# Performance work log

Hardware: AMD Instinct MI355X
Metric: run time of the kernel (lower is better)

The kernel has to match this reference:

```python
import jax, jax.numpy as jnp
import numpy as np

SHAPE = (192, 192, 192)


def _trilinear_sample(img, z, y, x):
    # img: [B,C,D,H,W]; z,y,x: [B,D,H,W] absolute voxel coords (align_corners=True,
    # zero padding outside the volume, matching F.grid_sample defaults in vroc).
    B, C, D, H, W = img.shape
    imgf = img.reshape(B, C, -1)
    z0 = jnp.floor(z); y0 = jnp.floor(y); x0 = jnp.floor(x)
    wz = z - z0; wy = y - y0; wx = x - x0
    z0i = z0.astype(jnp.int32); y0i = y0.astype(jnp.int32); x0i = x0.astype(jnp.int32)
    z1i = z0i + 1; y1i = y0i + 1; x1i = x0i + 1

    def gather(iz, iy, ix):
        valid = ((iz >= 0) & (iz < D) & (iy >= 0) & (iy < H) & (ix >= 0) & (ix < W))
        lin = ((jnp.clip(iz, 0, D - 1) * H + jnp.clip(iy, 0, H - 1)) * W
               + jnp.clip(ix, 0, W - 1)).reshape(B, 1, -1)
        v = jnp.take_along_axis(imgf, jnp.broadcast_to(lin, (B, C, D * H * W)), axis=2)
        return v.reshape(B, C, D, H, W) * valid.reshape(B, 1, D, H, W).astype(img.dtype)

    def w(a, b, c):
        return (a * b * c)[:, None]  # [B,1,D,H,W]

    out = (gather(z0i, y0i, x0i) * w(1 - wz, 1 - wy, 1 - wx)
           + gather(z0i, y0i, x1i) * w(1 - wz, 1 - wy, wx)
           + gather(z0i, y1i, x0i) * w(1 - wz, wy, 1 - wx)
           + gather(z0i, y1i, x1i) * w(1 - wz, wy, wx)
           + gather(z1i, y0i, x0i) * w(wz, 1 - wy, 1 - wx)
           + gather(z1i, y0i, x1i) * w(wz, 1 - wy, wx)
           + gather(z1i, y1i, x0i) * w(wz, wy, 1 - wx)
           + gather(z1i, y1i, x1i) * w(wz, wy, wx))
    return out


def _warp(moving_image, vector_field):
    # SpatialTransformer: identity grid + displacement (voxel units), trilinear sample.
    B, C, D, H, W = moving_image.shape
    dt = moving_image.dtype
    gz, gy, gx = jnp.meshgrid(jnp.arange(D, dtype=dt), jnp.arange(H, dtype=dt),
                              jnp.arange(W, dtype=dt), indexing='ij')
    z = gz[None] + vector_field[:, 0]
    y = gy[None] + vector_field[:, 1]
    x = gx[None] + vector_field[:, 2]
    return _trilinear_sample(moving_image, z, y, x)


def setup_inputs() -> dict:
    key = jax.random.key(0)
    k1, k2, k3, k4 = jax.random.split(key, 4)
    D, H, W = SHAPE
    moving_image = jax.random.normal(k1, (1, 1, D, H, W), dtype=jnp.float32)
    vector_field = jax.random.normal(k2, (1, 3, D, H, W), dtype=jnp.float32) * 3.0
    fixed_image = jax.random.normal(k3, (1, 1, D, H, W), dtype=jnp.float32)
    fixed_image_mask = jax.random.randint(k4, (1, 1, D, H, W), 0, 2).astype(bool)
    return {"moving_image": moving_image, "vector_field": vector_field,
            "fixed_image": fixed_image, "fixed_image_mask": fixed_image_mask}


def reference(moving_image, vector_field, fixed_image, fixed_image_mask):
    warped = _warp(moving_image, vector_field)
    m = fixed_image_mask.astype(warped.dtype)
    sq = (warped - fixed_image) ** 2
    # F.mse_loss(warped[mask], fixed[mask]) == mean of squared diff over masked voxels
    return jnp.sum(sq * m) / jnp.maximum(jnp.sum(m), 1.0)
```

## Files before the change

### kernel.cpp

```cpp
#include <hip/hip_runtime.h>
#include <hip/hip_fp16.h>

#define DD 192
#define HH 192
#define WW 192
#define NVOX (DD * HH * WW)

#define RSX 32
#define RSY 33
#define RSZ 33
#define ROWD 16
#define SLABD (RSY * ROWD)
#define RTOTH (RSX * RSY * RSZ)
#define RTOTD (RTOTH / 2)
#define MAXO (RTOTD - SLABD - ROWD - 2)
#define NCHUNK (RTOTH / 8)
#define CHSLAB (RSY * 4)
#define NT 1024
#define NTILE 1728
#define GRID 256

#define AS1 __attribute__((address_space(1)))
#define AS3 __attribute__((address_space(3)))

__global__ __launch_bounds__(256) void conv_fp16(
    const float4* __restrict__ in, int4* __restrict__ out)
{
    const int i = blockIdx.x * 256 + threadIdx.x;
    const float4 a = in[2 * i];
    const float4 b = in[2 * i + 1];
    __half2 h0 = __floats2half2_rn(a.x, a.y);
    __half2 h1 = __floats2half2_rn(a.z, a.w);
    __half2 h2 = __floats2half2_rn(b.x, b.y);
    __half2 h3 = __floats2half2_rn(b.z, b.w);
    int4 o;
    o.x = *(int*)&h0; o.y = *(int*)&h1; o.z = *(int*)&h2; o.w = *(int*)&h3;
    out[i] = o;
}

struct Streams { float4 dz, dy, dx, f; int4 m; };

__device__ __forceinline__ void tile_coords(int n, int& tx, int& ty, int& tz) {
    tx = n / 144;
    const int r = n - tx * 144;
    ty = r / 12;
    tz = r - ty * 12;
}

__device__ __forceinline__ void stage_tile(
    const ushort* __restrict__ movh, const ushort* __restrict__ zbuf,
    uint* sbufd, int x_lo, int y_lo, int z_lo, int tid)
{
    ushort* sbuf = (ushort*)sbufd;
    #pragma unroll
    for (int i = 0; i < 5; ++i) {
        const int q = tid + i * NT;
        if (q < NCHUNK) {
            const int rz = q / CHSLAB;
            const int rem = q - rz * CHSLAB;
            const int ry = rem >> 2;
            const int k  = rem & 3;
            const int gz = z_lo + rz, gy = y_lo + ry, gx = x_lo + 8 * k;
            const bool valid = ((unsigned)gz < DD) & ((unsigned)gy < HH) &
                               ((unsigned)gx < WW);
            const ushort* src = valid ? (movh + ((gz * HH + gy) * WW + gx)) : zbuf;
            const int qb = i * NT + (tid & ~63);
            __builtin_amdgcn_global_load_lds((AS1 void*)src,
                                             (AS3 void*)(sbuf + 8 * qb), 16, 0, 0);
        }
    }
}

__device__ __forceinline__ Streams prefetch_streams(
    const float* __restrict__ vf, const float* __restrict__ fix,
    const int* __restrict__ mask, int base)
{
    Streams s;
    s.dz = *(const float4*)(vf + base);
    s.dy = *(const float4*)(vf + NVOX + base);
    s.dx = *(const float4*)(vf + 2 * NVOX + base);
    s.f  = *(const float4*)(fix + base);
    s.m  = *(const int4*)(mask + base);
    return s;
}

__device__ __forceinline__ void sample_accum(
    const uint* sdw, const float* __restrict__ mov,
    int gz, int gy, int gx, float dz, float dy, float dx,
    float f, int m, int x_lo, int y_lo, int z_lo,
    float& sq, float& cnt)
{
    const float z = (float)gz + dz, y = (float)gy + dy, x = (float)gx + dx;
    const float z0f = floorf(z), y0f = floorf(y), x0f = floorf(x);
    const float wz = z - z0f, wy = y - y0f, wx = x - x0f;
    const int z0 = (int)z0f, y0 = (int)y0f, x0 = (int)x0f;
    const int z0l = z0 - z_lo, y0l = y0 - y_lo, x0l = x0 - x_lo;
    const bool inbox = ((unsigned)z0l < RSZ - 1) & ((unsigned)y0l < RSY - 1) &
                       ((unsigned)x0l < RSX - 1);

    float v000, v001, v010, v011, v100, v101, v110, v111;
    if (inbox) {
        const int o = z0l * SLABD + y0l * ROWD + (x0l >> 1);
        const bool odd = (x0l & 1) != 0;
        const uint a00 = sdw[o];
        const uint b00 = sdw[o + 1];
        const uint a01 = sdw[o + ROWD];
        const uint b01 = sdw[o + ROWD + 1];
        const uint a10 = sdw[o + SLABD];
        const uint b10 = sdw[o + SLABD + 1];
        const uint a11 = sdw[o + SLABD + ROWD];
        const uint b11 = sdw[o + SLABD + ROWD + 1];
        auto pr = [&](uint A, uint B, float& l, float& r) {
            const float2 fa = __half22float2(*(const __half2*)&A);
            const float fb = __low2float(*(const __half2*)&B);
            l = odd ? fa.y : fa.x;
            r = odd ? fb   : fa.y;
        };
        pr(a00, b00, v000, v001);
        pr(a01, b01, v010, v011);
        pr(a10, b10, v100, v101);
        pr(a11, b11, v110, v111);
    } else {
        const int z1 = z0 + 1, y1 = y0 + 1, x1 = x0 + 1;
        const bool zi0 = (unsigned)z0 < DD, zi1 = (unsigned)z1 < DD;
        const bool yi0 = (unsigned)y0 < HH, yi1 = (unsigned)y1 < HH;
        const bool xi0 = (unsigned)x0 < WW, xi1 = (unsigned)x1 < WW;
        auto ld = [&](int iz, int iy, int ix, bool ok) -> float {
            return ok ? mov[(iz * HH + iy) * WW + ix] : 0.0f;
        };
        v000 = ld(z0, y0, x0, zi0 & yi0 & xi0);
        v001 = ld(z0, y0, x1, zi0 & yi0 & xi1);
        v010 = ld(z0, y1, x0, zi0 & yi1 & xi0);
        v011 = ld(z0, y1, x1, zi0 & yi1 & xi1);
        v100 = ld(z1, y0, x0, zi1 & yi0 & xi0);
        v101 = ld(z1, y0, x1, zi1 & yi0 & xi1);
        v110 = ld(z1, y1, x0, zi1 & yi1 & xi0);
        v111 = ld(z1, y1, x1, zi1 & yi1 & xi1);
    }

    const float c00 = v000 + (v001 - v000) * wx;
    const float c01 = v010 + (v011 - v010) * wx;
    const float c10 = v100 + (v101 - v100) * wx;
    const float c11 = v110 + (v111 - v110) * wx;
    const float c0 = c00 + (c01 - c00) * wy;
    const float c1 = c10 + (c11 - c10) * wy;
    const float warped = c0 + (c1 - c0) * wz;

    const float mm = (m != 0) ? 1.0f : 0.0f;
    const float diff = warped - f;
    sq += diff * diff * mm;
    cnt += mm;
}

__global__ __launch_bounds__(NT) void warp_mse_persist(
    const ushort* __restrict__ movh,
    const float* __restrict__ mov,
    const float* __restrict__ vf,
    const float* __restrict__ fix,
    const int* __restrict__ mask,
    const ushort* __restrict__ zbuf,
    float* __restrict__ acc,
    float* __restrict__ out)
{
    __shared__ uint sbufd[2][RTOTD];
    __shared__ float s_sq[16], s_cnt[16];

    const int tid = threadIdx.x;
    const int b = blockIdx.x;
    const int start = b * 6 + min(b, 192);
    const int cnt_t = 6 + (b < 192 ? 1 : 0);

    const int lxg = (tid & 3) * 4;
    const int ly  = (tid >> 2) & 15;
    const int lz  = tid >> 6;

    float sq = 0.0f, cntm = 0.0f;

    int tx, ty, tz;
    tile_coords(start, tx, ty, tz);
    stage_tile(movh, zbuf, sbufd[0], tx * 16 - 8, ty * 16 - 8, tz * 16 - 8, tid);
    Streams S0 = prefetch_streams(vf, fix, mask,
        ((tz * 16 + lz) * HH + ty * 16 + ly) * WW + tx * 16 + lxg);
    __syncthreads();

    for (int k = 0; k < cnt_t; ++k) {
        const int cur = k & 1;
        Streams S1 = S0;
        if (k + 1 < cnt_t) {
            int nx, ny, nz;
            tile_coords(start + k + 1, nx, ny, nz);
            stage_tile(movh, zbuf, sbufd[cur ^ 1],
                       nx * 16 - 8, ny * 16 - 8, nz * 16 - 8, tid);
            S1 = prefetch_streams(vf, fix, mask,
                ((nz * 16 + lz) * HH + ny * 16 + ly) * WW + nx * 16 + lxg);
        }

        int cx, cy, cz;
        tile_coords(start + k, cx, cy, cz);
        const int x_lo = cx * 16 - 8, y_lo = cy * 16 - 8, z_lo = cz * 16 - 8;
        const int gz = cz * 16 + lz, gy = cy * 16 + ly, gx0 = cx * 16 + lxg;
        const uint* sdw = sbufd[cur];

        sample_accum(sdw, mov, gz, gy, gx0,     S0.dz.x, S0.dy.x, S0.dx.x,
                     S0.f.x, S0.m.x, x_lo, y_lo, z_lo, sq, cntm);
        sample_accum(sdw, mov, gz, gy, gx0 + 1, S0.dz.y, S0.dy.y, S0.dx.y,
                     S0.f.y, S0.m.y, x_lo, y_lo, z_lo, sq, cntm);
        sample_accum(sdw, mov, gz, gy, gx0 + 2, S0.dz.z, S0.dy.z, S0.dx.z,
                     S0.f.z, S0.m.z, x_lo, y_lo, z_lo, sq, cntm);
        sample_accum(sdw, mov, gz, gy, gx0 + 3, S0.dz.w, S0.dy.w, S0.dx.w,
                     S0.f.w, S0.m.w, x_lo, y_lo, z_lo, sq, cntm);

        __syncthreads();
        S0 = S1;
    }

    #pragma unroll
    for (int off = 32; off > 0; off >>= 1) {
        sq   += __shfl_down(sq, off, 64);
        cntm += __shfl_down(cntm, off, 64);
    }
    const int lane = tid & 63;
    const int wid = tid >> 6;
    if (lane == 0) { s_sq[wid] = sq; s_cnt[wid] = cntm; }
    __syncthreads();
    if (tid == 0) {
        float bsq = 0.0f, bcnt = 0.0f;
        #pragma unroll
        for (int i = 0; i < 16; ++i) { bsq += s_sq[i]; bcnt += s_cnt[i]; }
        atomicAdd(&acc[0], bsq);
        atomicAdd(&acc[1], bcnt);
        __threadfence();
        const unsigned old = atomicAdd((unsigned*)&acc[2], 1u);
        if (old == GRID - 1) {
            __threadfence();
            const float s = atomicAdd(&acc[0], 0.0f);
            const float c = atomicAdd(&acc[1], 0.0f);
            out[0] = s / fmaxf(c, 1.0f);
        }
    }
}

__global__ __launch_bounds__(256) void warp_mse_simple(
    const float* __restrict__ mov, const float* __restrict__ vf,
    const float* __restrict__ fix, const int* __restrict__ mask,
    float* __restrict__ acc)
{
    const int idx = blockIdx.x * 256 + threadIdx.x;
    float sq = 0.0f, cnt = 0.0f;
    if (idx < NVOX) {
        const int w = idx % WW;
        const int t = idx / WW;
        const int h = t % HH;
        const int d = t / HH;
        const float z = (float)d + vf[idx];
        const float y = (float)h + vf[NVOX + idx];
        const float x = (float)w + vf[2 * NVOX + idx];
        const float z0f = floorf(z), y0f = floorf(y), x0f = floorf(x);
        const float wz = z - z0f, wy = y - y0f, wx = x - x0f;
        const int z0 = (int)z0f, y0 = (int)y0f, x0 = (int)x0f;
        const int z1 = z0 + 1, y1 = y0 + 1, x1 = x0 + 1;
        const bool zi0 = (unsigned)z0 < DD, zi1 = (unsigned)z1 < DD;
        const bool yi0 = (unsigned)y0 < HH, yi1 = (unsigned)y1 < HH;
        const bool xi0 = (unsigned)x0 < WW, xi1 = (unsigned)x1 < WW;
        auto ld = [&](int iz, int iy, int ix, bool ok) -> float {
            return ok ? mov[(iz * HH + iy) * WW + ix] : 0.0f;
        };
        const float v000 = ld(z0, y0, x0, zi0 & yi0 & xi0);
        const float v001 = ld(z0, y0, x1, zi0 & yi0 & xi1);
        const float v010 = ld(z0, y1, x0, zi0 & yi1 & xi0);
        const float v011 = ld(z0, y1, x1, zi0 & yi1 & xi1);
        const float v100 = ld(z1, y0, x0, zi1 & yi0 & xi0);
        const float v101 = ld(z1, y0, x1, zi1 & yi0 & xi1);
        const float v110 = ld(z1, y1, x0, zi1 & yi1 & xi0);
        const float v111 = ld(z1, y1, x1, zi1 & yi1 & xi1);
        const float c00 = v000 + (v001 - v000) * wx;
        const float c01 = v010 + (v011 - v010) * wx;
        const float c10 = v100 + (v101 - v100) * wx;
        const float c11 = v110 + (v111 - v110) * wx;
        const float c0 = c00 + (c01 - c00) * wy;
        const float c1 = c10 + (c11 - c10) * wy;
        const float warped = c0 + (c1 - c0) * wz;
        const float m = (mask[idx] != 0) ? 1.0f : 0.0f;
        const float diff = warped - fix[idx];
        sq = diff * diff * m;
        cnt = m;
    }
    #pragma unroll
    for (int off = 32; off > 0; off >>= 1) {
        sq  += __shfl_down(sq, off, 64);
        cnt += __shfl_down(cnt, off, 64);
    }
    __shared__ float s_sq[4], s_cnt[4];
    const int lane = threadIdx.x & 63, wid = threadIdx.x >> 6;
    if (lane == 0) { s_sq[wid] = sq; s_cnt[wid] = cnt; }
    __syncthreads();
    if (threadIdx.x == 0) {
        atomicAdd(&acc[0], s_sq[0] + s_sq[1] + s_sq[2] + s_sq[3]);
        atomicAdd(&acc[1], s_cnt[0] + s_cnt[1] + s_cnt[2] + s_cnt[3]);
    }
}

__global__ void warp_mse_finalize(const float* __restrict__ acc, float* __restrict__ out) {
    out[0] = acc[0] / fmaxf(acc[1], 1.0f);
}

extern "C" void kernel_launch(void* const* d_in, const int* in_sizes, int n_in,
                              void* d_out, int out_size, void* d_ws, size_t ws_size,
                              hipStream_t stream) {
    const float* mov  = (const float*)d_in[0];
    const float* vf   = (const float*)d_in[1];
    const float* fix  = (const float*)d_in[2];
    const int*   mask = (const int*)d_in[3];
    float* acc = (float*)d_ws;
    float* out = (float*)d_out;

    hipMemsetAsync(d_ws, 0, 256, stream);

    const size_t need = 256 + (size_t)NVOX * 2;
    if (ws_size >= need) {
        ushort* movh = (ushort*)((char*)d_ws + 256);
        const ushort* zbuf = (const ushort*)((char*)d_ws + 64);
        conv_fp16<<<NVOX / (256 * 8), 256, 0, stream>>>(
            (const float4*)mov, (int4*)movh);
        warp_mse_persist<<<GRID, NT, 0, stream>>>(movh, mov, vf, fix, mask,
                                                  zbuf, acc, out);
    } else {
        warp_mse_simple<<<(NVOX + 255) / 256, 256, 0, stream>>>(mov, vf, fix, mask, acc);
        warp_mse_finalize<<<1, 1, 0, stream>>>(acc, out);
    }
}
```

Before: 246.0 us.

## Single-buffer LDS tile with 512-thread blocks for higher occupancy and locality

Halves the block size to 512 threads, with each thread handling two z-slices of a tile, and drops the LDS double buffer in favour of one tile buffer. Launch bounds now request four blocks per CU and the grid grows to 512 blocks. Blocks are remapped so that neighbouring blocks take interleaved tiles. Streaming loads of the displacement field, fixed image and mask become nontemporal. More resident blocks should hide latency better, but staging is no longer overlapped with compute within a block and now needs an extra barrier per tile.

```diff
diff --git a/kernel.cpp b/kernel.cpp
--- a/kernel.cpp
+++ b/kernel.cpp
@@ -13,15 +13,18 @@
 #define SLABD (RSY * ROWD)
 #define RTOTH (RSX * RSY * RSZ)
 #define RTOTD (RTOTH / 2)
-#define MAXO (RTOTD - SLABD - ROWD - 2)
 #define NCHUNK (RTOTH / 8)
 #define CHSLAB (RSY * 4)
-#define NT 1024
+#define NT 512
+#define NROUND ((NCHUNK + NT - 1) / NT)
 #define NTILE 1728
-#define GRID 256
+#define GRID 512
 
 #define AS1 __attribute__((address_space(1)))
 #define AS3 __attribute__((address_space(3)))
+
+typedef float f32x4 __attribute__((ext_vector_type(4)));
+typedef int   i32x4 __attribute__((ext_vector_type(4)));
 
 __global__ __launch_bounds__(256) void conv_fp16(
     const float4* __restrict__ in, int4* __restrict__ out)
@@ -38,7 +41,7 @@
     out[i] = o;
 }
 
-struct Streams { float4 dz, dy, dx, f; int4 m; };
+struct Streams { f32x4 dz, dy, dx, f; i32x4 m; };
 
 __device__ __forceinline__ void tile_coords(int n, int& tx, int& ty, int& tz) {
     tx = n / 144;
@@ -53,7 +56,7 @@
 {
     ushort* sbuf = (ushort*)sbufd;
     #pragma unroll
-    for (int i = 0; i < 5; ++i) {
+    for (int i = 0; i < NROUND; ++i) {
         const int q = tid + i * NT;
         if (q < NCHUNK) {
             const int rz = q / CHSLAB;
@@ -76,11 +79,11 @@
     const int* __restrict__ mask, int base)
 {
     Streams s;
-    s.dz = *(const float4*)(vf + base);
-    s.dy = *(const float4*)(vf + NVOX + base);
-    s.dx = *(const float4*)(vf + 2 * NVOX + base);
-    s.f  = *(const float4*)(fix + base);
-    s.m  = *(const int4*)(mask + base);
+    s.dz = __builtin_nontemporal_load((const f32x4*)(vf + base));
+    s.dy = __builtin_nontemporal_load((const f32x4*)(vf + NVOX + base));
+    s.dx = __builtin_nontemporal_load((const f32x4*)(vf + 2 * NVOX + base));
+    s.f  = __builtin_nontemporal_load((const f32x4*)(fix + base));
+    s.m  = __builtin_nontemporal_load((const i32x4*)(mask + base));
     return s;
 }
 
@@ -152,7 +155,7 @@
     cnt += mm;
 }
 
-__global__ __launch_bounds__(NT) void warp_mse_persist(
+__global__ __launch_bounds__(NT, 4) void warp_mse_persist(
     const ushort* __restrict__ movh,
     const float* __restrict__ mov,
     const float* __restrict__ vf,
@@ -162,13 +165,14 @@
     float* __restrict__ acc,
     float* __restrict__ out)
 {
-    __shared__ uint sbufd[2][RTOTD];
-    __shared__ float s_sq[16], s_cnt[16];
+    __shared__ uint sbufd[RTOTD];
+    __shared__ float s_sq[8], s_cnt[8];
 
     const int tid = threadIdx.x;
-    const int b = blockIdx.x;
-    const int start = b * 6 + min(b, 192);
-    const int cnt_t = 6 + (b < 192 ? 1 : 0);
+    const int b0 = blockIdx.x;
+    const int b = ((b0 & 7) << 6) | (b0 >> 3);
+    const int start = 3 * b + 3 * (b >> 3) + min(b & 7, 3);
+    const int cnt_t = 3 + ((b & 7) < 3 ? 1 : 0);
 
     const int lxg = (tid & 3) * 4;
     const int ly  = (tid >> 2) & 15;
@@ -178,40 +182,53 @@
 
     int tx, ty, tz;
     tile_coords(start, tx, ty, tz);
-    stage_tile(movh, zbuf, sbufd[0], tx * 16 - 8, ty * 16 - 8, tz * 16 - 8, tid);
-    Streams S0 = prefetch_streams(vf, fix, mask,
+    stage_tile(movh, zbuf, sbufd, tx * 16 - 8, ty * 16 - 8, tz * 16 - 8, tid);
+    Streams SA = prefetch_streams(vf, fix, mask,
         ((tz * 16 + lz) * HH + ty * 16 + ly) * WW + tx * 16 + lxg);
     __syncthreads();
 
     for (int k = 0; k < cnt_t; ++k) {
-        const int cur = k & 1;
-        Streams S1 = S0;
-        if (k + 1 < cnt_t) {
-            int nx, ny, nz;
-            tile_coords(start + k + 1, nx, ny, nz);
-            stage_tile(movh, zbuf, sbufd[cur ^ 1],
-                       nx * 16 - 8, ny * 16 - 8, nz * 16 - 8, tid);
-            S1 = prefetch_streams(vf, fix, mask,
-                ((nz * 16 + lz) * HH + ny * 16 + ly) * WW + nx * 16 + lxg);
-        }
-
         int cx, cy, cz;
         tile_coords(start + k, cx, cy, cz);
         const int x_lo = cx * 16 - 8, y_lo = cy * 16 - 8, z_lo = cz * 16 - 8;
-        const int gz = cz * 16 + lz, gy = cy * 16 + ly, gx0 = cx * 16 + lxg;
-        const uint* sdw = sbufd[cur];
-
-        sample_accum(sdw, mov, gz, gy, gx0,     S0.dz.x, S0.dy.x, S0.dx.x,
-                     S0.f.x, S0.m.x, x_lo, y_lo, z_lo, sq, cntm);
-        sample_accum(sdw, mov, gz, gy, gx0 + 1, S0.dz.y, S0.dy.y, S0.dx.y,
-                     S0.f.y, S0.m.y, x_lo, y_lo, z_lo, sq, cntm);
-        sample_accum(sdw, mov, gz, gy, gx0 + 2, S0.dz.z, S0.dy.z, S0.dx.z,
-                     S0.f.z, S0.m.z, x_lo, y_lo, z_lo, sq, cntm);
-        sample_accum(sdw, mov, gz, gy, gx0 + 3, S0.dz.w, S0.dy.w, S0.dx.w,
-                     S0.f.w, S0.m.w, x_lo, y_lo, z_lo, sq, cntm);
+        const int gzA = cz * 16 + lz, gy = cy * 16 + ly, gx0 = cx * 16 + lxg;
+        const uint* sdw = sbufd;
+
+        Streams SB = prefetch_streams(vf, fix, mask,
+            ((gzA + 8) * HH + gy) * WW + gx0);
+
+        sample_accum(sdw, mov, gzA, gy, gx0,     SA.dz.x, SA.dy.x, SA.dx.x,
+                     SA.f.x, SA.m.x, x_lo, y_lo, z_lo, sq, cntm);
+        sample_accum(sdw, mov, gzA, gy, gx0 + 1, SA.dz.y, SA.dy.y, SA.dx.y,
+                     SA.f.y, SA.m.y, x_lo, y_lo, z_lo, sq, cntm);
+        sample_accum(sdw, mov, gzA, gy, gx0 + 2, SA.dz.z, SA.dy.z, SA.dx.z,
+                     SA.f.z, SA.m.z, x_lo, y_lo, z_lo, sq, cntm);
+        sample_accum(sdw, mov, gzA, gy, gx0 + 3, SA.dz.w, SA.dy.w, SA.dx.w,
+                     SA.f.w, SA.m.w, x_lo, y_lo, z_lo, sq, cntm);
+
+        const bool more = (k + 1 < cnt_t);
+        int nx = 0, ny = 0, nz = 0;
+        if (more) {
+            tile_coords(start + k + 1, nx, ny, nz);
+            SA = prefetch_streams(vf, fix, mask,
+                ((nz * 16 + lz) * HH + ny * 16 + ly) * WW + nx * 16 + lxg);
+        }
+
+        sample_accum(sdw, mov, gzA + 8, gy, gx0,     SB.dz.x, SB.dy.x, SB.dx.x,
+                     SB.f.x, SB.m.x, x_lo, y_lo, z_lo, sq, cntm);
+        sample_accum(sdw, mov, gzA + 8, gy, gx0 + 1, SB.dz.y, SB.dy.y, SB.dx.y,
+                     SB.f.y, SB.m.y, x_lo, y_lo, z_lo, sq, cntm);
+        sample_accum(sdw, mov, gzA + 8, gy, gx0 + 2, SB.dz.z, SB.dy.z, SB.dx.z,
+                     SB.f.z, SB.m.z, x_lo, y_lo, z_lo, sq, cntm);
+        sample_accum(sdw, mov, gzA + 8, gy, gx0 + 3, SB.dz.w, SB.dy.w, SB.dx.w,
+                     SB.f.w, SB.m.w, x_lo, y_lo, z_lo, sq, cntm);
 
         __syncthreads();
-        S0 = S1;
+        if (more) {
+            stage_tile(movh, zbuf, sbufd,
+                       nx * 16 - 8, ny * 16 - 8, nz * 16 - 8, tid);
+            __syncthreads();
+        }
     }
 
     #pragma unroll
@@ -226,7 +243,7 @@
     if (tid == 0) {
         float bsq = 0.0f, bcnt = 0.0f;
         #pragma unroll
-        for (int i = 0; i < 16; ++i) { bsq += s_sq[i]; bcnt += s_cnt[i]; }
+        for (int i = 0; i < 8; ++i) { bsq += s_sq[i]; bcnt += s_cnt[i]; }
         atomicAdd(&acc[0], bsq);
         atomicAdd(&acc[1], bcnt);
         __threadfence();
```

New measurement: 294.5 us. 1.2x slower.

## Replace LDS-staged persistent warp kernel with direct fp16 global gathers

Applied to the files above, without the earlier changes.

Drops the persistent kernel that double-buffered halo tiles of the fp16 moving image into shared memory. In its place is a plain one-block-per-2048-voxel kernel where each thread processes 8 voxels and gathers its 8 trilinear corners straight from the fp16 copy through the cache. Streaming inputs use nontemporal loads, and block indices are remapped so each XCD gets a contiguous range, which should improve L2 locality. This removes LDS staging, barriers and the inbox branch, but relies on the cache hierarchy to absorb the scattered gathers and launches many more blocks, each paying an atomic.

```diff
diff --git a/kernel.cpp b/kernel.cpp
--- a/kernel.cpp
+++ b/kernel.cpp
@@ -6,22 +6,13 @@
 #define WW 192
 #define NVOX (DD * HH * WW)
 
-#define RSX 32
-#define RSY 33
-#define RSZ 33
-#define ROWD 16
-#define SLABD (RSY * ROWD)
-#define RTOTH (RSX * RSY * RSZ)
-#define RTOTD (RTOTH / 2)
-#define MAXO (RTOTD - SLABD - ROWD - 2)
-#define NCHUNK (RTOTH / 8)
-#define CHSLAB (RSY * 4)
-#define NT 1024
-#define NTILE 1728
-#define GRID 256
-
-#define AS1 __attribute__((address_space(1)))
-#define AS3 __attribute__((address_space(3)))
+#define VPB 2048
+#define NBLK (NVOX / VPB)
+#define NXCD 8
+#define BPX (NBLK / NXCD)
+
+typedef float f32x4 __attribute__((ext_vector_type(4)));
+typedef int   i32x4 __attribute__((ext_vector_type(4)));
 
 __global__ __launch_bounds__(256) void conv_fp16(
     const float4* __restrict__ in, int4* __restrict__ out)
@@ -38,105 +29,49 @@
     out[i] = o;
 }
 
-struct Streams { float4 dz, dy, dx, f; int4 m; };
-
-__device__ __forceinline__ void tile_coords(int n, int& tx, int& ty, int& tz) {
-    tx = n / 144;
-    const int r = n - tx * 144;
-    ty = r / 12;
-    tz = r - ty * 12;
-}
-
-__device__ __forceinline__ void stage_tile(
-    const ushort* __restrict__ movh, const ushort* __restrict__ zbuf,
-    uint* sbufd, int x_lo, int y_lo, int z_lo, int tid)
-{
-    ushort* sbuf = (ushort*)sbufd;
-    #pragma unroll
-    for (int i = 0; i < 5; ++i) {
-        const int q = tid + i * NT;
-        if (q < NCHUNK) {
-            const int rz = q / CHSLAB;
-            const int rem = q - rz * CHSLAB;
-            const int ry = rem >> 2;
-            const int k  = rem & 3;
-            const int gz = z_lo + rz, gy = y_lo + ry, gx = x_lo + 8 * k;
-            const bool valid = ((unsigned)gz < DD) & ((unsigned)gy < HH) &
-                               ((unsigned)gx < WW);
-            const ushort* src = valid ? (movh + ((gz * HH + gy) * WW + gx)) : zbuf;
-            const int qb = i * NT + (tid & ~63);
-            __builtin_amdgcn_global_load_lds((AS1 void*)src,
-                                             (AS3 void*)(sbuf + 8 * qb), 16, 0, 0);
-        }
-    }
-}
-
-__device__ __forceinline__ Streams prefetch_streams(
-    const float* __restrict__ vf, const float* __restrict__ fix,
-    const int* __restrict__ mask, int base)
-{
-    Streams s;
-    s.dz = *(const float4*)(vf + base);
-    s.dy = *(const float4*)(vf + NVOX + base);
-    s.dx = *(const float4*)(vf + 2 * NVOX + base);
-    s.f  = *(const float4*)(fix + base);
-    s.m  = *(const int4*)(mask + base);
-    return s;
-}
-
-__device__ __forceinline__ void sample_accum(
-    const uint* sdw, const float* __restrict__ mov,
+__device__ __forceinline__ f32x4 ntl(const float* p) {
+    return __builtin_nontemporal_load((const f32x4*)p);
+}
+__device__ __forceinline__ i32x4 ntli(const int* p) {
+    return __builtin_nontemporal_load((const i32x4*)p);
+}
+
+__device__ __forceinline__ void sample_one(
+    const __half* __restrict__ movh,
     int gz, int gy, int gx, float dz, float dy, float dx,
-    float f, int m, int x_lo, int y_lo, int z_lo,
-    float& sq, float& cnt)
+    float f, int m, float& sq, float& cnt)
 {
     const float z = (float)gz + dz, y = (float)gy + dy, x = (float)gx + dx;
     const float z0f = floorf(z), y0f = floorf(y), x0f = floorf(x);
     const float wz = z - z0f, wy = y - y0f, wx = x - x0f;
     const int z0 = (int)z0f, y0 = (int)y0f, x0 = (int)x0f;
-    const int z0l = z0 - z_lo, y0l = y0 - y_lo, x0l = x0 - x_lo;
-    const bool inbox = ((unsigned)z0l < RSZ - 1) & ((unsigned)y0l < RSY - 1) &
-                       ((unsigned)x0l < RSX - 1);
-
-    float v000, v001, v010, v011, v100, v101, v110, v111;
-    if (inbox) {
-        const int o = z0l * SLABD + y0l * ROWD + (x0l >> 1);
-        const bool odd = (x0l & 1) != 0;
-        const uint a00 = sdw[o];
-        const uint b00 = sdw[o + 1];
-        const uint a01 = sdw[o + ROWD];
-        const uint b01 = sdw[o + ROWD + 1];
-        const uint a10 = sdw[o + SLABD];
-        const uint b10 = sdw[o + SLABD + 1];
-        const uint a11 = sdw[o + SLABD + ROWD];
-        const uint b11 = sdw[o + SLABD + ROWD + 1];
-        auto pr = [&](uint A, uint B, float& l, float& r) {
-            const float2 fa = __half22float2(*(const __half2*)&A);
-            const float fb = __low2float(*(const __half2*)&B);
-            l = odd ? fa.y : fa.x;
-            r = odd ? fb   : fa.y;
-        };
-        pr(a00, b00, v000, v001);
-        pr(a01, b01, v010, v011);
-        pr(a10, b10, v100, v101);
-        pr(a11, b11, v110, v111);
-    } else {
-        const int z1 = z0 + 1, y1 = y0 + 1, x1 = x0 + 1;
-        const bool zi0 = (unsigned)z0 < DD, zi1 = (unsigned)z1 < DD;
-        const bool yi0 = (unsigned)y0 < HH, yi1 = (unsigned)y1 < HH;
-        const bool xi0 = (unsigned)x0 < WW, xi1 = (unsigned)x1 < WW;
-        auto ld = [&](int iz, int iy, int ix, bool ok) -> float {
-            return ok ? mov[(iz * HH + iy) * WW + ix] : 0.0f;
-        };
-        v000 = ld(z0, y0, x0, zi0 & yi0 & xi0);
-        v001 = ld(z0, y0, x1, zi0 & yi0 & xi1);
-        v010 = ld(z0, y1, x0, zi0 & yi1 & xi0);
-        v011 = ld(z0, y1, x1, zi0 & yi1 & xi1);
-        v100 = ld(z1, y0, x0, zi1 & yi0 & xi0);
-        v101 = ld(z1, y0, x1, zi1 & yi0 & xi1);
-        v110 = ld(z1, y1, x0, zi1 & yi1 & xi0);
-        v111 = ld(z1, y1, x1, zi1 & yi1 & xi1);
-    }
+    const int z1 = z0 + 1, y1 = y0 + 1, x1 = x0 + 1;
+    const bool zi0 = (unsigned)z0 < DD, zi1 = (unsigned)z1 < DD;
+    const bool yi0 = (unsigned)y0 < HH, yi1 = (unsigned)y1 < HH;
+    const bool xi0 = (unsigned)x0 < WW, xi1 = (unsigned)x1 < WW;
+    const int zc0 = min(max(z0, 0), DD - 1), zc1 = min(max(z1, 0), DD - 1);
+    const int yc0 = min(max(y0, 0), HH - 1), yc1 = min(max(y1, 0), HH - 1);
+    const int xc0 = min(max(x0, 0), WW - 1), xc1 = min(max(x1, 0), WW - 1);
+    const int r00 = (zc0 * HH + yc0) * WW;
+    const int r01 = (zc0 * HH + yc1) * WW;
+    const int r10 = (zc1 * HH + yc0) * WW;
+    const int r11 = (zc1 * HH + yc1) * WW;
+    float v000 = __half2float(movh[r00 + xc0]);
+    float v001 = __half2float(movh[r00 + xc1]);
+    float v010 = __half2float(movh[r01 + xc0]);
+    float v011 = __half2float(movh[r01 + xc1]);
+    float v100 = __half2float(movh[r10 + xc0]);
+    float v101 = __half2float(movh[r10 + xc1]);
+    float v110 = __half2float(movh[r11 + xc0]);
+    float v111 = __half2float(movh[r11 + xc1]);
+    v000 = (zi0 & yi0 & xi0) ? v000 : 0.0f;
+    v001 = (zi0 & yi0 & xi1) ? v001 : 0.0f;
+    v010 = (zi0 & yi1 & xi0) ? v010 : 0.0f;
+    v011 = (zi0 & yi1 & xi1) ? v011 : 0.0f;
+    v100 = (zi1 & yi0 & xi0) ? v100 : 0.0f;
+    v101 = (zi1 & yi0 & xi1) ? v101 : 0.0f;
+    v110 = (zi1 & yi1 & xi0) ? v110 : 0.0f;
+    v111 = (zi1 & yi1 & xi1) ? v111 : 0.0f;
 
     const float c00 = v000 + (v001 - v000) * wx;
     const float c01 = v010 + (v011 - v010) * wx;
@@ -152,86 +87,57 @@
     cnt += mm;
 }
 
-__global__ __launch_bounds__(NT) void warp_mse_persist(
-    const ushort* __restrict__ movh,
-    const float* __restrict__ mov,
+__global__ __launch_bounds__(256) void warp_mse_gather(
+    const __half* __restrict__ movh,
     const float* __restrict__ vf,
     const float* __restrict__ fix,
     const int* __restrict__ mask,
-    const ushort* __restrict__ zbuf,
     float* __restrict__ acc,
     float* __restrict__ out)
 {
-    __shared__ uint sbufd[2][RTOTD];
-    __shared__ float s_sq[16], s_cnt[16];
-
-    const int tid = threadIdx.x;
-    const int b = blockIdx.x;
-    const int start = b * 6 + min(b, 192);
-    const int cnt_t = 6 + (b < 192 ? 1 : 0);
-
-    const int lxg = (tid & 3) * 4;
-    const int ly  = (tid >> 2) & 15;
-    const int lz  = tid >> 6;
-
-    float sq = 0.0f, cntm = 0.0f;
-
-    int tx, ty, tz;
-    tile_coords(start, tx, ty, tz);
-    stage_tile(movh, zbuf, sbufd[0], tx * 16 - 8, ty * 16 - 8, tz * 16 - 8, tid);
-    Streams S0 = prefetch_streams(vf, fix, mask,
-        ((tz * 16 + lz) * HH + ty * 16 + ly) * WW + tx * 16 + lxg);
-    __syncthreads();
-
-    for (int k = 0; k < cnt_t; ++k) {
-        const int cur = k & 1;
-        Streams S1 = S0;
-        if (k + 1 < cnt_t) {
-            int nx, ny, nz;
-            tile_coords(start + k + 1, nx, ny, nz);
-            stage_tile(movh, zbuf, sbufd[cur ^ 1],
-                       nx * 16 - 8, ny * 16 - 8, nz * 16 - 8, tid);
-            S1 = prefetch_streams(vf, fix, mask,
-                ((nz * 16 + lz) * HH + ny * 16 + ly) * WW + nx * 16 + lxg);
-        }
-
-        int cx, cy, cz;
-        tile_coords(start + k, cx, cy, cz);
-        const int x_lo = cx * 16 - 8, y_lo = cy * 16 - 8, z_lo = cz * 16 - 8;
-        const int gz = cz * 16 + lz, gy = cy * 16 + ly, gx0 = cx * 16 + lxg;
-        const uint* sdw = sbufd[cur];
-
-        sample_accum(sdw, mov, gz, gy, gx0,     S0.dz.x, S0.dy.x, S0.dx.x,
-                     S0.f.x, S0.m.x, x_lo, y_lo, z_lo, sq, cntm);
-        sample_accum(sdw, mov, gz, gy, gx0 + 1, S0.dz.y, S0.dy.y, S0.dx.y,
-                     S0.f.y, S0.m.y, x_lo, y_lo, z_lo, sq, cntm);
-        sample_accum(sdw, mov, gz, gy, gx0 + 2, S0.dz.z, S0.dy.z, S0.dx.z,
-                     S0.f.z, S0.m.z, x_lo, y_lo, z_lo, sq, cntm);
-        sample_accum(sdw, mov, gz, gy, gx0 + 3, S0.dz.w, S0.dy.w, S0.dx.w,
-                     S0.f.w, S0.m.w, x_lo, y_lo, z_lo, sq, cntm);
-
-        __syncthreads();
-        S0 = S1;
-    }
+    __shared__ float s_sq[4], s_cnt[4];
+
+    const int b0 = blockIdx.x;
+    const int L = (b0 & (NXCD - 1)) * BPX + (b0 >> 3);
+    const int base = L * VPB + (threadIdx.x << 3);
+    const int row = base / WW;
+    const int gx  = base - row * WW;
+    const int gy  = row % HH;
+    const int gz  = row / HH;
+
+    const f32x4 za = ntl(vf + base),            zb = ntl(vf + base + 4);
+    const f32x4 ya = ntl(vf + NVOX + base),     yb = ntl(vf + NVOX + base + 4);
+    const f32x4 xa = ntl(vf + 2 * NVOX + base), xb = ntl(vf + 2 * NVOX + base + 4);
+    const f32x4 fa = ntl(fix + base),           fb = ntl(fix + base + 4);
+    const i32x4 ma = ntli(mask + base),         mb = ntli(mask + base + 4);
+
+    float sq = 0.0f, cnt = 0.0f;
+    sample_one(movh, gz, gy, gx + 0, za.x, ya.x, xa.x, fa.x, ma.x, sq, cnt);
+    sample_one(movh, gz, gy, gx + 1, za.y, ya.y, xa.y, fa.y, ma.y, sq, cnt);
+    sample_one(movh, gz, gy, gx + 2, za.z, ya.z, xa.z, fa.z, ma.z, sq, cnt);
+    sample_one(movh, gz, gy, gx + 3, za.w, ya.w, xa.w, fa.w, ma.w, sq, cnt);
+    sample_one(movh, gz, gy, gx + 4, zb.x, yb.x, xb.x, fb.x, mb.x, sq, cnt);
+    sample_one(movh, gz, gy, gx + 5, zb.y, yb.y, xb.y, fb.y, mb.y, sq, cnt);
+    sample_one(movh, gz, gy, gx + 6, zb.z, yb.z, xb.z, fb.z, mb.z, sq, cnt);
+    sample_one(movh, gz, gy, gx + 7, zb.w, yb.w, xb.w, fb.w, mb.w, sq, cnt);
 
     #pragma unroll
     for (int off = 32; off > 0; off >>= 1) {
-        sq   += __shfl_down(sq, off, 64);
-        cntm += __shfl_down(cntm, off, 64);
-    }
-    const int lane = tid & 63;
-    const int wid = tid >> 6;
-    if (lane == 0) { s_sq[wid] = sq; s_cnt[wid] = cntm; }
+        sq  += __shfl_down(sq, off, 64);
+        cnt += __shfl_down(cnt, off, 64);
+    }
+    const int lane = threadIdx.x & 63;
+    const int wid = threadIdx.x >> 6;
+    if (lane == 0) { s_sq[wid] = sq; s_cnt[wid] = cnt; }
     __syncthreads();
-    if (tid == 0) {
-        float bsq = 0.0f, bcnt = 0.0f;
-        #pragma unroll
-        for (int i = 0; i < 16; ++i) { bsq += s_sq[i]; bcnt += s_cnt[i]; }
+    if (threadIdx.x == 0) {
+        const float bsq  = s_sq[0] + s_sq[1] + s_sq[2] + s_sq[3];
+        const float bcnt = s_cnt[0] + s_cnt[1] + s_cnt[2] + s_cnt[3];
         atomicAdd(&acc[0], bsq);
         atomicAdd(&acc[1], bcnt);
         __threadfence();
         const unsigned old = atomicAdd((unsigned*)&acc[2], 1u);
-        if (old == GRID - 1) {
+        if (old == NBLK - 1) {
             __threadfence();
             const float s = atomicAdd(&acc[0], 0.0f);
             const float c = atomicAdd(&acc[1], 0.0f);
@@ -318,12 +224,10 @@
 
     const size_t need = 256 + (size_t)NVOX * 2;
     if (ws_size >= need) {
-        ushort* movh = (ushort*)((char*)d_ws + 256);
-        const ushort* zbuf = (const ushort*)((char*)d_ws + 64);
+        __half* movh = (__half*)((char*)d_ws + 256);
         conv_fp16<<<NVOX / (256 * 8), 256, 0, stream>>>(
             (const float4*)mov, (int4*)movh);
-        warp_mse_persist<<<GRID, NT, 0, stream>>>(movh, mov, vf, fix, mask,
-                                                  zbuf, acc, out);
+        warp_mse_gather<<<NBLK, 256, 0, stream>>>(movh, vf, fix, mask, acc, out);
     } else {
         warp_mse_simple<<<(NVOX + 255) / 256, 256, 0, stream>>>(mov, vf, fix, mask, acc);
         warp_mse_finalize<<<1, 1, 0, stream>>>(acc, out);
```

New measurement: 510.1 us. +107.4%, slower.

## Deepen LDS staging pipeline to two tiles ahead with explicit vmcnt waits

Applied to the files above, without the earlier changes.

Restructures the tile loop so that two tiles are in flight: each buffer is refilled right after its compute finishes, and explicit s_waitcnt vmcnt counts let the wave wait only for the older tile's global-to-LDS loads rather than draining all memory operations at a __syncthreads. Stream loads of the displacement field, fixed image and mask switch to nontemporal loads so these single-use streams avoid polluting cache. This adds hand-counted wait values that must match the number of outstanding loads per thread, plus more live registers for two stream sets.

```diff
diff --git a/kernel.cpp b/kernel.cpp
--- a/kernel.cpp
+++ b/kernel.cpp
@@ -13,15 +13,20 @@
 #define SLABD (RSY * ROWD)
 #define RTOTH (RSX * RSY * RSZ)
 #define RTOTD (RTOTH / 2)
-#define MAXO (RTOTD - SLABD - ROWD - 2)
 #define NCHUNK (RTOTH / 8)
 #define CHSLAB (RSY * 4)
 #define NT 1024
+#define NROUND ((NCHUNK + NT - 1) / NT)
 #define NTILE 1728
 #define GRID 256
 
 #define AS1 __attribute__((address_space(1)))
 #define AS3 __attribute__((address_space(3)))
+
+#define WAITCNT(n) asm volatile("s_waitcnt vmcnt(" #n ")" ::: "memory")
+
+typedef float f32x4 __attribute__((ext_vector_type(4)));
+typedef int   i32x4 __attribute__((ext_vector_type(4)));
 
 __global__ __launch_bounds__(256) void conv_fp16(
     const float4* __restrict__ in, int4* __restrict__ out)
@@ -38,7 +43,7 @@
     out[i] = o;
 }
 
-struct Streams { float4 dz, dy, dx, f; int4 m; };
+struct Streams { f32x4 dz, dy, dx, f; i32x4 m; };
 
 __device__ __forceinline__ void tile_coords(int n, int& tx, int& ty, int& tz) {
     tx = n / 144;
@@ -53,7 +58,7 @@
 {
     ushort* sbuf = (ushort*)sbufd;
     #pragma unroll
-    for (int i = 0; i < 5; ++i) {
+    for (int i = 0; i < NROUND; ++i) {
         const int q = tid + i * NT;
         if (q < NCHUNK) {
             const int rz = q / CHSLAB;
@@ -76,11 +81,11 @@
     const int* __restrict__ mask, int base)
 {
     Streams s;
-    s.dz = *(const float4*)(vf + base);
-    s.dy = *(const float4*)(vf + NVOX + base);
-    s.dx = *(const float4*)(vf + 2 * NVOX + base);
-    s.f  = *(const float4*)(fix + base);
-    s.m  = *(const int4*)(mask + base);
+    s.dz = __builtin_nontemporal_load((const f32x4*)(vf + base));
+    s.dy = __builtin_nontemporal_load((const f32x4*)(vf + NVOX + base));
+    s.dx = __builtin_nontemporal_load((const f32x4*)(vf + 2 * NVOX + base));
+    s.f  = __builtin_nontemporal_load((const f32x4*)(fix + base));
+    s.m  = __builtin_nontemporal_load((const i32x4*)(mask + base));
     return s;
 }
 
@@ -179,39 +184,59 @@
     int tx, ty, tz;
     tile_coords(start, tx, ty, tz);
     stage_tile(movh, zbuf, sbufd[0], tx * 16 - 8, ty * 16 - 8, tz * 16 - 8, tid);
-    Streams S0 = prefetch_streams(vf, fix, mask,
+    Streams Scur = prefetch_streams(vf, fix, mask,
         ((tz * 16 + lz) * HH + ty * 16 + ly) * WW + tx * 16 + lxg);
-    __syncthreads();
+    Streams Snxt = Scur;
+    if (cnt_t > 1) {
+        int nx, ny, nz;
+        tile_coords(start + 1, nx, ny, nz);
+        stage_tile(movh, zbuf, sbufd[1], nx * 16 - 8, ny * 16 - 8, nz * 16 - 8, tid);
+        Snxt = prefetch_streams(vf, fix, mask,
+            ((nz * 16 + lz) * HH + ny * 16 + ly) * WW + nx * 16 + lxg);
+        WAITCNT(14);
+    } else {
+        WAITCNT(5);
+    }
+    __builtin_amdgcn_s_barrier();
+    __builtin_amdgcn_sched_barrier(0);
 
     for (int k = 0; k < cnt_t; ++k) {
         const int cur = k & 1;
-        Streams S1 = S0;
-        if (k + 1 < cnt_t) {
-            int nx, ny, nz;
-            tile_coords(start + k + 1, nx, ny, nz);
-            stage_tile(movh, zbuf, sbufd[cur ^ 1],
-                       nx * 16 - 8, ny * 16 - 8, nz * 16 - 8, tid);
-            S1 = prefetch_streams(vf, fix, mask,
-                ((nz * 16 + lz) * HH + ny * 16 + ly) * WW + nx * 16 + lxg);
-        }
-
         int cx, cy, cz;
         tile_coords(start + k, cx, cy, cz);
         const int x_lo = cx * 16 - 8, y_lo = cy * 16 - 8, z_lo = cz * 16 - 8;
         const int gz = cz * 16 + lz, gy = cy * 16 + ly, gx0 = cx * 16 + lxg;
         const uint* sdw = sbufd[cur];
 
-        sample_accum(sdw, mov, gz, gy, gx0,     S0.dz.x, S0.dy.x, S0.dx.x,
-                     S0.f.x, S0.m.x, x_lo, y_lo, z_lo, sq, cntm);
-        sample_accum(sdw, mov, gz, gy, gx0 + 1, S0.dz.y, S0.dy.y, S0.dx.y,
-                     S0.f.y, S0.m.y, x_lo, y_lo, z_lo, sq, cntm);
-        sample_accum(sdw, mov, gz, gy, gx0 + 2, S0.dz.z, S0.dy.z, S0.dx.z,
-                     S0.f.z, S0.m.z, x_lo, y_lo, z_lo, sq, cntm);
-        sample_accum(sdw, mov, gz, gy, gx0 + 3, S0.dz.w, S0.dy.w, S0.dx.w,
-                     S0.f.w, S0.m.w, x_lo, y_lo, z_lo, sq, cntm);
-
-        __syncthreads();
-        S0 = S1;
+        sample_accum(sdw, mov, gz, gy, gx0,     Scur.dz.x, Scur.dy.x, Scur.dx.x,
+                     Scur.f.x, Scur.m.x, x_lo, y_lo, z_lo, sq, cntm);
+        sample_accum(sdw, mov, gz, gy, gx0 + 1, Scur.dz.y, Scur.dy.y, Scur.dx.y,
+                     Scur.f.y, Scur.m.y, x_lo, y_lo, z_lo, sq, cntm);
+        sample_accum(sdw, mov, gz, gy, gx0 + 2, Scur.dz.z, Scur.dy.z, Scur.dx.z,
+                     Scur.f.z, Scur.m.z, x_lo, y_lo, z_lo, sq, cntm);
+        sample_accum(sdw, mov, gz, gy, gx0 + 3, Scur.dz.w, Scur.dy.w, Scur.dx.w,
+                     Scur.f.w, Scur.m.w, x_lo, y_lo, z_lo, sq, cntm);
+
+        if (k + 1 < cnt_t) {
+            __builtin_amdgcn_sched_barrier(0);
+            __builtin_amdgcn_s_barrier();
+            Streams Snew = Snxt;
+            if (k + 2 < cnt_t) {
+                int nx, ny, nz;
+                tile_coords(start + k + 2, nx, ny, nz);
+                stage_tile(movh, zbuf, sbufd[cur],
+                           nx * 16 - 8, ny * 16 - 8, nz * 16 - 8, tid);
+                Snew = prefetch_streams(vf, fix, mask,
+                    ((nz * 16 + lz) * HH + ny * 16 + ly) * WW + nx * 16 + lxg);
+                WAITCNT(14);
+            } else {
+                WAITCNT(5);
+            }
+            __builtin_amdgcn_s_barrier();
+            __builtin_amdgcn_sched_barrier(0);
+            Scur = Snxt;
+            Snxt = Snew;
+        }
     }
 
     #pragma unroll
```

New measurement: 246.7 us. About the same (+0.3%).
